# Kernel tuning notes

Measured on AMD Instinct MI355X. Metric: run time of the kernel, lower is better.

Reference implementation:

```python
import jax, jax.numpy as jnp
import numpy as np
from jax import lax

K = 5  # SCNN_KERNEL_LENGTH
PAD = K - 1
PAD_L = PAD // 2
PAD_R = PAD - PAD_L


def setup_inputs() -> dict:
    key = jax.random.key(0)
    k1, k2 = jax.random.split(key)
    B, H, W, C = 16, 256, 256, 32
    inputs = jax.random.normal(k1, (B, H, W, C), dtype=jnp.float32)
    # keras 'random_uniform' init is small; scale randn similarly to keep relu chain stable
    w = jax.random.normal(k2, (C, K, 1, C), dtype=jnp.float32) * 0.05
    b = jnp.zeros((C,), dtype=jnp.float32)
    return {"inputs": inputs, "w": w, "b": b}


def _mvcnn_down(inputs, w, b):
    # inputs: [B,H,W,C]; w: [C,K,1,C] (tf filter: [fh=C, fw=K, in=1, out=C])
    # The tf conv of the transposed row [B,C,W,1] with this filter is exactly a
    # 1D conv over W mixing all C input channels:
    #   out[b,x,o] = sum_{k,c} row_pad[b, x+k, c] * w[c,k,0,o]
    kernel = jnp.transpose(w[:, :, 0, :], (1, 0, 2))  # [K, C_in, C_out]

    def conv_row(x):  # x: [B,W,C] -> [B,W,C]
        return lax.conv_general_dilated(
            x, kernel, window_strides=(1,), padding=[(PAD_L, PAD_R)],
            dimension_numbers=("NWC", "WIO", "NWC"))

    rows = jnp.transpose(inputs, (1, 0, 2, 3))  # [H,B,W,C]

    def step(carry, row):
        # row i of the evolving state = original row + relu-conv result of row i-1
        x = row + carry
        r = jax.nn.relu(conv_row(x) + b)
        return r, r

    init = jnp.zeros_like(rows[0])
    _, out_rows = lax.scan(step, init, rows)  # [H,B,W,C]
    return jnp.transpose(out_rows, (1, 0, 2, 3))  # [B,H,W,C]


def reference(inputs, w, b):
    return _mvcnn_down(inputs, w, b)
```

## Files before the change

### kernel.cpp

```cpp
#include <hip/hip_runtime.h>
#include <stdint.h>

typedef _Float16 f16;
typedef _Float16 f16x2 __attribute__((ext_vector_type(2)));
typedef _Float16 f16x8 __attribute__((ext_vector_type(8)));
typedef float f32x4 __attribute__((ext_vector_type(4)));

#define NB 16
#define NH 256
#define NW 256
#define NC 32
#define NK 5

#define CW 16
#define GC 16
#define XSTR 40
#define XROWS 52

#define FLAG_STRIDE 16
#define MAIL_BASE 4096
#define MAIL_WORDS 256

__device__ __forceinline__ void lds_barrier() {
  asm volatile("s_waitcnt lgkmcnt(0)\n\ts_barrier" ::: "memory");
}

__global__ __launch_bounds__(192, 1)
void mvcnn_down_mb(const float* __restrict__ in, const float* __restrict__ wt,
                   const float* __restrict__ bias, float* __restrict__ out,
                   uint32_t* __restrict__ ws) {
  __shared__ __align__(16) f16 xpad[2][XROWS * XSTR];

  const int bid  = blockIdx.x;
  const int b    = bid & 15;
  const int ck   = bid >> 4;
  const int t    = threadIdx.x;
  const int lane = t & 63;
  const int wv   = t >> 6;
  const int n16  = lane & 15;
  const int q    = lane >> 4;

  const bool act = (wv == 1) || (wv == 0 ? (ck > 0) : (ck < GC - 1));

  f16x8 bfrag[NK][2];
  #pragma unroll
  for (int tap = 0; tap < NK; ++tap) {
    #pragma unroll
    for (int nt = 0; nt < 2; ++nt) {
      f16x8 f;
      #pragma unroll
      for (int j = 0; j < 8; ++j) {
        int cch = q * 4 + (j >> 1) + (j & 1) * 16;
        f[j] = (f16)wt[(cch * NK + tap) * NC + nt * 16 + n16];
      }
      bfrag[tap][nt] = f;
    }
  }
  const float bias0 = bias[n16];
  const float bias1 = bias[16 + n16];

  for (int i = t; i < 2 * XROWS * XSTR; i += 192) (&xpad[0][0])[i] = (f16)0.f;
  __syncthreads();

  const float* inb  = in  + (size_t)b * NH * NW * NC;
  float*       outb = out + (size_t)b * NH * NW * NC;

  const int wo0   = wv * 16 + q * 4;
  const int gcol0 = ck * CW - 16 + wo0;
  const int arow  = wv * 16 + n16;

  uint32_t* flags = ws;
  uint32_t* mail  = ws + MAIL_BASE;
  const int midx  = (q * 4) * 16 + n16;

  float pf0[8], pf1[8];
  auto load_in_row = [&](int h1, float (&pf)[8]) {
    if (!act) return;
    const float* rp = inb + (size_t)h1 * NW * NC;
    #pragma unroll
    for (int r = 0; r < 4; ++r) {
      int g = gcol0 + r;
      pf[2 * r]     = rp[g * NC + n16];
      pf[2 * r + 1] = rp[g * NC + 16 + n16];
    }
  };

  if (act) {
    #pragma unroll
    for (int r = 0; r < 4; ++r) {
      int g = gcol0 + r;
      f16x2 v;
      v[0] = (f16)inb[g * NC + n16];
      v[1] = (f16)inb[g * NC + 16 + n16];
      *(f16x2*)(&xpad[0][(wo0 + r + 2) * XSTR + 2 * n16]) = v;
    }
  }
  load_in_row(1, pf0);
  load_in_row(2, pf1);
  __syncthreads();

  auto body = [&](const int h, float (&pf)[8], f16* xp_cur, f16* xp_nxt) {
    if (h > 0 && (h & 7) == 0) {
      const uint32_t s  = (uint32_t)(h >> 3);
      const int slot    = (int)(s & 1);
      if ((wv == 0 && ck > 0) || (wv == 2 && ck < GC - 1)) {
        const int nb = (wv == 0) ? (bid - GC) : (bid + GC);
        if (lane == 0) {
          while (__hip_atomic_load(&flags[nb * FLAG_STRIDE],
                                   __ATOMIC_RELAXED, __HIP_MEMORY_SCOPE_AGENT) < s)
            __builtin_amdgcn_s_sleep(2);
        }
        asm volatile("" ::: "memory");
        const uint32_t* mb = mail + ((size_t)nb * 2 + slot) * MAIL_WORDS;
        #pragma unroll
        for (int r = 0; r < 4; ++r) {
          uint32_t u = __hip_atomic_load(&mb[midx + r * 16],
                                         __ATOMIC_RELAXED, __HIP_MEMORY_SCOPE_AGENT);
          *(uint32_t*)(&xp_cur[(wo0 + r + 2) * XSTR + 2 * n16]) = u;
        }
      }
      lds_barrier();
    }

    f32x4 acc0 = {0.f, 0.f, 0.f, 0.f};
    f32x4 acc1 = {0.f, 0.f, 0.f, 0.f};
    #pragma unroll
    for (int tap = 0; tap < NK; ++tap) {
      f16x8 af = *(const f16x8*)(xp_cur + (arow + tap) * XSTR + q * 8);
      acc0 = __builtin_amdgcn_mfma_f32_16x16x32_f16(af, bfrag[tap][0], acc0, 0, 0, 0);
      acc1 = __builtin_amdgcn_mfma_f32_16x16x32_f16(af, bfrag[tap][1], acc1, 0, 0, 0);
    }

    float* orow = outb + (size_t)h * NW * NC;
    uint32_t sb[4] = {0, 0, 0, 0};
    #pragma unroll
    for (int r = 0; r < 4; ++r) {
      float y0 = acc0[r] + bias0; y0 = y0 > 0.f ? y0 : 0.f;
      float y1 = acc1[r] + bias1; y1 = y1 > 0.f ? y1 : 0.f;
      if (wv == 1) {
        int g = gcol0 + r;
        orow[g * NC + n16]      = y0;
        orow[g * NC + 16 + n16] = y1;
      }
      if (h < NH - 1 && act) {
        f16x2 v;
        v[0] = (f16)(pf[2 * r]     + y0);
        v[1] = (f16)(pf[2 * r + 1] + y1);
        *(f16x2*)(&xp_nxt[(wo0 + r + 2) * XSTR + 2 * n16]) = v;
        sb[r] = __builtin_bit_cast(uint32_t, v);
      }
    }

    if (((h + 1) & 7) == 0 && (h + 1) < NH && wv == 1) {
      const uint32_t s = (uint32_t)((h + 1) >> 3);
      const int slot   = (int)(s & 1);
      uint32_t* mb = mail + ((size_t)bid * 2 + slot) * MAIL_WORDS;
      #pragma unroll
      for (int r = 0; r < 4; ++r)
        __hip_atomic_store(&mb[midx + r * 16], sb[r],
                           __ATOMIC_RELAXED, __HIP_MEMORY_SCOPE_AGENT);
      asm volatile("s_waitcnt vmcnt(0)" ::: "memory");
      if (lane == 0)
        __hip_atomic_store(&flags[bid * FLAG_STRIDE], s,
                           __ATOMIC_RELAXED, __HIP_MEMORY_SCOPE_AGENT);
    }

    if (h + 3 < NH) load_in_row(h + 3, pf);
    lds_barrier();
  };

  f16* xA = &xpad[0][0];
  f16* xB = &xpad[1][0];
  for (int h = 0; h < NH; h += 2) {
    body(h,     pf0, xA, xB);
    body(h + 1, pf1, xB, xA);
  }
}

__global__ void reset_flags(uint32_t* ws) {
  ws[blockIdx.x * 256 + threadIdx.x] = 0;
}

__global__ __launch_bounds__(1024, 4)
void mvcnn_down(const float* __restrict__ in, const float* __restrict__ wt,
                const float* __restrict__ bias, float* __restrict__ out) {
  __shared__ __align__(16) f16 xpad[2][260 * XSTR];

  const int b    = blockIdx.x;
  const int t    = threadIdx.x;
  const int lane = t & 63;
  const int wv   = t >> 6;
  const int n16  = lane & 15;
  const int q    = lane >> 4;

  f16x8 bfrag[NK][2];
  #pragma unroll
  for (int tap = 0; tap < NK; ++tap) {
    #pragma unroll
    for (int nt = 0; nt < 2; ++nt) {
      f16x8 f;
      #pragma unroll
      for (int j = 0; j < 8; ++j) {
        int cch = q * 4 + (j >> 1) + (j & 1) * 16;
        f[j] = (f16)wt[(cch * NK + tap) * NC + nt * 16 + n16];
      }
      bfrag[tap][nt] = f;
    }
  }
  const float bias0 = bias[n16];
  const float bias1 = bias[16 + n16];

  for (int i = t; i < 2 * 260 * XSTR; i += 1024) (&xpad[0][0])[i] = (f16)0.f;
  __syncthreads();

  const float* inb  = in  + (size_t)b * NH * NW * NC;
  float*       outb = out + (size_t)b * NH * NW * NC;

  const int wo0  = wv * 16 + q * 4;
  const int arow = wv * 16 + n16;

  float pf0[8], pf1[8];
  auto load_in_row = [&](int h1, float (&pf)[8]) {
    const float* rp = inb + (size_t)h1 * NW * NC;
    #pragma unroll
    for (int r = 0; r < 4; ++r) {
      int wo = wo0 + r;
      pf[2 * r]     = rp[wo * NC + n16];
      pf[2 * r + 1] = rp[wo * NC + 16 + n16];
    }
  };

  #pragma unroll
  for (int r = 0; r < 4; ++r) {
    int wo = wo0 + r;
    f16x2 v;
    v[0] = (f16)inb[wo * NC + n16];
    v[1] = (f16)inb[wo * NC + 16 + n16];
    *(f16x2*)(&xpad[0][(wo + 2) * XSTR + 2 * n16]) = v;
  }
  load_in_row(1, pf0);
  load_in_row(2, pf1);
  __syncthreads();

  auto body = [&](const int h, float (&pf)[8], const f16* xp_cur, f16* xp_nxt) {
    f32x4 acc0 = {0.f, 0.f, 0.f, 0.f};
    f32x4 acc1 = {0.f, 0.f, 0.f, 0.f};
    #pragma unroll
    for (int tap = 0; tap < NK; ++tap) {
      f16x8 af = *(const f16x8*)(xp_cur + (arow + tap) * XSTR + q * 8);
      acc0 = __builtin_amdgcn_mfma_f32_16x16x32_f16(af, bfrag[tap][0], acc0, 0, 0, 0);
      acc1 = __builtin_amdgcn_mfma_f32_16x16x32_f16(af, bfrag[tap][1], acc1, 0, 0, 0);
    }
    float* orow = outb + (size_t)h * NW * NC;
    #pragma unroll
    for (int r = 0; r < 4; ++r) {
      float y0 = acc0[r] + bias0; y0 = y0 > 0.f ? y0 : 0.f;
      float y1 = acc1[r] + bias1; y1 = y1 > 0.f ? y1 : 0.f;
      int wo = wo0 + r;
      orow[wo * NC + n16]      = y0;
      orow[wo * NC + 16 + n16] = y1;
      if (h < NH - 1) {
        f16x2 v;
        v[0] = (f16)(pf[2 * r]     + y0);
        v[1] = (f16)(pf[2 * r + 1] + y1);
        *(f16x2*)(&xp_nxt[(wo + 2) * XSTR + 2 * n16]) = v;
      }
    }
    if (h + 3 < NH) load_in_row(h + 3, pf);
    lds_barrier();
  };

  const f16* xA = &xpad[0][0];
  f16* xB = &xpad[1][0];
  for (int h = 0; h < NH; h += 2) {
    body(h,     pf0, xA, xB);
    body(h + 1, pf1, xB, (f16*)xA);
  }
}

extern "C" void kernel_launch(void* const* d_in, const int* in_sizes, int n_in,
                              void* d_out, int out_size, void* d_ws, size_t ws_size,
                              hipStream_t stream) {
  const float* in   = (const float*)d_in[0];
  const float* wt   = (const float*)d_in[1];
  const float* bias = (const float*)d_in[2];
  float* out = (float*)d_out;

  const size_t need = (size_t)(MAIL_BASE + 256 * 2 * MAIL_WORDS) * 4;
  if (d_ws != nullptr && ws_size >= need) {
    hipLaunchKernelGGL(reset_flags, dim3(16), dim3(256), 0, stream, (uint32_t*)d_ws);
    hipLaunchKernelGGL(mvcnn_down_mb, dim3(NB * GC), dim3(192), 0, stream,
                       in, wt, bias, out, (uint32_t*)d_ws);
  } else {
    hipLaunchKernelGGL(mvcnn_down, dim3(NB), dim3(1024), 0, stream,
                       in, wt, bias, out);
  }
}
```

Measured before the change: 377.5 us.

## Compute two rows per barrier with widened halo and key-tagged flags

Each even-row step now computes a wider halo of outputs (two extra MFMA tiles per wave), so the following odd row can be built entirely from data the same wave wrote. That removes one LDS barrier per pair of rows. LDS goes to triple buffering, and input prefetch is split into wide and narrow loads. Neighbour-exchange flags become per-slot tags derived from the step index, which removes the separate flag-reset kernel launch. In exchange the even rows do redundant boundary compute and the control logic is more complex.

Measured after the change: 936.8 us. 2.48x slower.

```diff
diff --git a/kernel.cpp b/kernel.cpp
--- a/kernel.cpp
+++ b/kernel.cpp
@@ -15,11 +15,13 @@
 #define CW 16
 #define GC 16
 #define XSTR 40
-#define XROWS 52
-
-#define FLAG_STRIDE 16
-#define MAIL_BASE 4096
+#define XROWS 56
+
+#define FLAG_U32 16
+#define NFLAGS (NB * GC * 2 * FLAG_U32)
+#define MAIL_BASE NFLAGS
 #define MAIL_WORDS 256
+#define KEYOF(k) (0x5EED0000u ^ (uint32_t)(k))
 
 __device__ __forceinline__ void lds_barrier() {
   asm volatile("s_waitcnt lgkmcnt(0)\n\ts_barrier" ::: "memory");
@@ -29,7 +31,7 @@
 void mvcnn_down_mb(const float* __restrict__ in, const float* __restrict__ wt,
                    const float* __restrict__ bias, float* __restrict__ out,
                    uint32_t* __restrict__ ws) {
-  __shared__ __align__(16) f16 xpad[2][XROWS * XSTR];
+  __shared__ __align__(16) f16 xpad[3][XROWS * XSTR];
 
   const int bid  = blockIdx.x;
   const int b    = bid & 15;
@@ -59,7 +61,7 @@
   const float bias0 = bias[n16];
   const float bias1 = bias[16 + n16];
 
-  for (int i = t; i < 2 * XROWS * XSTR; i += 192) (&xpad[0][0])[i] = (f16)0.f;
+  for (int i = t; i < 3 * XROWS * XSTR; i += 192) (&xpad[0][0])[i] = (f16)0.f;
   __syncthreads();
 
   const float* inb  = in  + (size_t)b * NH * NW * NC;
@@ -73,15 +75,36 @@
   uint32_t* mail  = ws + MAIL_BASE;
   const int midx  = (q * 4) * 16 + n16;
 
-  float pf0[8], pf1[8];
-  auto load_in_row = [&](int h1, float (&pf)[8]) {
-    if (!act) return;
+  float pW1[2][8], pW0[2][8], pN[2][8];
+
+  auto load_narrow = [&](int h1, float (&pf)[8]) {
+    if (!act || h1 >= NH) return;
     const float* rp = inb + (size_t)h1 * NW * NC;
     #pragma unroll
     for (int r = 0; r < 4; ++r) {
       int g = gcol0 + r;
       pf[2 * r]     = rp[g * NC + n16];
       pf[2 * r + 1] = rp[g * NC + 16 + n16];
+    }
+  };
+  auto load_wide = [&](int h1, float (&pT1)[8], float (&pT0)[8]) {
+    if (!act || h1 >= NH) return;
+    const float* rp = inb + (size_t)h1 * NW * NC;
+    #pragma unroll
+    for (int r = 0; r < 4; ++r) {
+      int g1 = gcol0 + 2 + r;
+      int gc = g1 < NW ? g1 : NW - 1;
+      pT1[2 * r]     = rp[gc * NC + n16];
+      pT1[2 * r + 1] = rp[gc * NC + 16 + n16];
+    }
+    if (q == 0) {
+      #pragma unroll
+      for (int r = 0; r < 4; ++r) {
+        int g0 = gcol0 - 2 + r;
+        int gc = g0 > 0 ? g0 : 0;
+        pT0[2 * r]     = rp[gc * NC + n16];
+        pT0[2 * r + 1] = rp[gc * NC + 16 + n16];
+      }
     }
   };
 
@@ -92,93 +115,147 @@
       f16x2 v;
       v[0] = (f16)inb[g * NC + n16];
       v[1] = (f16)inb[g * NC + 16 + n16];
-      *(f16x2*)(&xpad[0][(wo0 + r + 2) * XSTR + 2 * n16]) = v;
-    }
-  }
-  load_in_row(1, pf0);
-  load_in_row(2, pf1);
+      *(f16x2*)(&xpad[0][(wo0 + r + 4) * XSTR + 2 * n16]) = v;
+    }
+  }
+  load_wide(1, pW1[0], pW0[0]);
+  load_narrow(2, pN[0]);
   __syncthreads();
 
-  auto body = [&](const int h, float (&pf)[8], f16* xp_cur, f16* xp_nxt) {
+  auto body_even = [&](const int h, float (&pT1)[8], float (&pT0)[8],
+                       f16* xp_cur, f16* xp_nxt) {
     if (h > 0 && (h & 7) == 0) {
-      const uint32_t s  = (uint32_t)(h >> 3);
-      const int slot    = (int)(s & 1);
+      const int k = h >> 3;
+      const int ms = k & 1;
       if ((wv == 0 && ck > 0) || (wv == 2 && ck < GC - 1)) {
         const int nb = (wv == 0) ? (bid - GC) : (bid + GC);
         if (lane == 0) {
-          while (__hip_atomic_load(&flags[nb * FLAG_STRIDE],
-                                   __ATOMIC_RELAXED, __HIP_MEMORY_SCOPE_AGENT) < s)
-            __builtin_amdgcn_s_sleep(2);
+          while (__hip_atomic_load(&flags[(nb * 2 + ms) * FLAG_U32],
+                                   __ATOMIC_RELAXED, __HIP_MEMORY_SCOPE_AGENT)
+                 != KEYOF(k))
+            __builtin_amdgcn_s_sleep(1);
         }
         asm volatile("" ::: "memory");
-        const uint32_t* mb = mail + ((size_t)nb * 2 + slot) * MAIL_WORDS;
+        const uint32_t* mb = mail + ((size_t)nb * 2 + ms) * MAIL_WORDS;
         #pragma unroll
         for (int r = 0; r < 4; ++r) {
           uint32_t u = __hip_atomic_load(&mb[midx + r * 16],
                                          __ATOMIC_RELAXED, __HIP_MEMORY_SCOPE_AGENT);
-          *(uint32_t*)(&xp_cur[(wo0 + r + 2) * XSTR + 2 * n16]) = u;
+          *(uint32_t*)(&xp_cur[(wo0 + r + 4) * XSTR + 2 * n16]) = u;
         }
       }
       lds_barrier();
     }
 
-    f32x4 acc0 = {0.f, 0.f, 0.f, 0.f};
-    f32x4 acc1 = {0.f, 0.f, 0.f, 0.f};
+    f32x4 a00 = {bias0, bias0, bias0, bias0};
+    f32x4 a01 = {bias1, bias1, bias1, bias1};
+    f32x4 a10 = a00, a11 = a01;
     #pragma unroll
     for (int tap = 0; tap < NK; ++tap) {
-      f16x8 af = *(const f16x8*)(xp_cur + (arow + tap) * XSTR + q * 8);
+      f16x8 f0 = *(const f16x8*)(xp_cur + (arow + tap) * XSTR + q * 8);
+      f16x8 f1 = *(const f16x8*)(xp_cur + (arow + tap + 4) * XSTR + q * 8);
+      a00 = __builtin_amdgcn_mfma_f32_16x16x32_f16(f0, bfrag[tap][0], a00, 0, 0, 0);
+      a01 = __builtin_amdgcn_mfma_f32_16x16x32_f16(f0, bfrag[tap][1], a01, 0, 0, 0);
+      a10 = __builtin_amdgcn_mfma_f32_16x16x32_f16(f1, bfrag[tap][0], a10, 0, 0, 0);
+      a11 = __builtin_amdgcn_mfma_f32_16x16x32_f16(f1, bfrag[tap][1], a11, 0, 0, 0);
+    }
+
+    float* orow = outb + (size_t)h * NW * NC;
+    #pragma unroll
+    for (int r = 0; r < 4; ++r) {
+      float y00 = fmaxf(a00[r], 0.f), y01 = fmaxf(a01[r], 0.f);
+      float y10 = fmaxf(a10[r], 0.f), y11 = fmaxf(a11[r], 0.f);
+      const int g1 = gcol0 + 2 + r;
+      const int g0 = gcol0 - 2 + r;
+      if (wv == 1) {
+        if (q * 4 + r <= 13) {
+          orow[g1 * NC + n16]      = y10;
+          orow[g1 * NC + 16 + n16] = y11;
+        }
+        if (q == 0 && r >= 2) {
+          orow[g0 * NC + n16]      = y00;
+          orow[g0 * NC + 16 + n16] = y01;
+        }
+      }
+      if (h < NH - 1 && act) {
+        if ((unsigned)g1 < NW) {
+          f16x2 v;
+          v[0] = (f16)(pT1[2 * r]     + y10);
+          v[1] = (f16)(pT1[2 * r + 1] + y11);
+          *(f16x2*)(&xp_nxt[(wv * 16 + 6 + q * 4 + r) * XSTR + 2 * n16]) = v;
+        }
+        if (q == 0 && (unsigned)g0 < NW) {
+          f16x2 v;
+          v[0] = (f16)(pT0[2 * r]     + y00);
+          v[1] = (f16)(pT0[2 * r + 1] + y01);
+          *(f16x2*)(&xp_nxt[(wv * 16 + 2 + r) * XSTR + 2 * n16]) = v;
+        }
+      }
+    }
+  };
+
+  auto body_odd = [&](const int h, float (&pf)[8], f16* xp_cur, f16* xp_nxt) {
+    f32x4 acc0 = {bias0, bias0, bias0, bias0};
+    f32x4 acc1 = {bias1, bias1, bias1, bias1};
+    #pragma unroll
+    for (int tap = 0; tap < NK; ++tap) {
+      f16x8 af = *(const f16x8*)(xp_cur + (arow + tap + 2) * XSTR + q * 8);
       acc0 = __builtin_amdgcn_mfma_f32_16x16x32_f16(af, bfrag[tap][0], acc0, 0, 0, 0);
       acc1 = __builtin_amdgcn_mfma_f32_16x16x32_f16(af, bfrag[tap][1], acc1, 0, 0, 0);
     }
 
-    float* orow = outb + (size_t)h * NW * NC;
     uint32_t sb[4] = {0, 0, 0, 0};
-    #pragma unroll
-    for (int r = 0; r < 4; ++r) {
-      float y0 = acc0[r] + bias0; y0 = y0 > 0.f ? y0 : 0.f;
-      float y1 = acc1[r] + bias1; y1 = y1 > 0.f ? y1 : 0.f;
-      if (wv == 1) {
-        int g = gcol0 + r;
-        orow[g * NC + n16]      = y0;
-        orow[g * NC + 16 + n16] = y1;
-      }
+    float y0v[4], y1v[4];
+    #pragma unroll
+    for (int r = 0; r < 4; ++r) {
+      float y0 = fmaxf(acc0[r], 0.f);
+      float y1 = fmaxf(acc1[r], 0.f);
+      y0v[r] = y0; y1v[r] = y1;
       if (h < NH - 1 && act) {
         f16x2 v;
         v[0] = (f16)(pf[2 * r]     + y0);
         v[1] = (f16)(pf[2 * r + 1] + y1);
-        *(f16x2*)(&xp_nxt[(wo0 + r + 2) * XSTR + 2 * n16]) = v;
+        *(f16x2*)(&xp_nxt[(wo0 + r + 4) * XSTR + 2 * n16]) = v;
         sb[r] = __builtin_bit_cast(uint32_t, v);
       }
     }
 
     if (((h + 1) & 7) == 0 && (h + 1) < NH && wv == 1) {
-      const uint32_t s = (uint32_t)((h + 1) >> 3);
-      const int slot   = (int)(s & 1);
-      uint32_t* mb = mail + ((size_t)bid * 2 + slot) * MAIL_WORDS;
+      const int k = (h + 1) >> 3;
+      const int ms = k & 1;
+      uint32_t* mb = mail + ((size_t)bid * 2 + ms) * MAIL_WORDS;
       #pragma unroll
       for (int r = 0; r < 4; ++r)
         __hip_atomic_store(&mb[midx + r * 16], sb[r],
                            __ATOMIC_RELAXED, __HIP_MEMORY_SCOPE_AGENT);
       asm volatile("s_waitcnt vmcnt(0)" ::: "memory");
       if (lane == 0)
-        __hip_atomic_store(&flags[bid * FLAG_STRIDE], s,
+        __hip_atomic_store(&flags[(bid * 2 + ms) * FLAG_U32], KEYOF(k),
                            __ATOMIC_RELAXED, __HIP_MEMORY_SCOPE_AGENT);
     }
 
-    if (h + 3 < NH) load_in_row(h + 3, pf);
+    if (wv == 1) {
+      float* orow = outb + (size_t)h * NW * NC;
+      #pragma unroll
+      for (int r = 0; r < 4; ++r) {
+        const int g = gcol0 + r;
+        orow[g * NC + n16]      = y0v[r];
+        orow[g * NC + 16 + n16] = y1v[r];
+      }
+    }
+  };
+
+  for (int h = 0; h < NH; h += 2) {
+    const int it = (h >> 1) & 1;
+    f16* bA = &xpad[h % 3][0];
+    f16* bB = &xpad[(h + 1) % 3][0];
+    f16* bC = &xpad[(h + 2) % 3][0];
+    body_even(h, pW1[it], pW0[it], bA, bB);
+    load_wide(h + 3, pW1[it ^ 1], pW0[it ^ 1]);
+    body_odd(h + 1, pN[it], bB, bC);
+    load_narrow(h + 4, pN[it ^ 1]);
     lds_barrier();
-  };
-
-  f16* xA = &xpad[0][0];
-  f16* xB = &xpad[1][0];
-  for (int h = 0; h < NH; h += 2) {
-    body(h,     pf0, xA, xB);
-    body(h + 1, pf1, xB, xA);
-  }
-}
-
-__global__ void reset_flags(uint32_t* ws) {
-  ws[blockIdx.x * 256 + threadIdx.x] = 0;
+  }
 }
 
 __global__ __launch_bounds__(1024, 4)
@@ -286,9 +363,8 @@
   const float* bias = (const float*)d_in[2];
   float* out = (float*)d_out;
 
-  const size_t need = (size_t)(MAIL_BASE + 256 * 2 * MAIL_WORDS) * 4;
+  const size_t need = (size_t)(NFLAGS + NB * GC * 2 * MAIL_WORDS) * 4;
   if (d_ws != nullptr && ws_size >= need) {
-    hipLaunchKernelGGL(reset_flags, dim3(16), dim3(256), 0, stream, (uint32_t*)d_ws);
     hipLaunchKernelGGL(mvcnn_down_mb, dim3(NB * GC), dim3(192), 0, stream,
                        in, wt, bias, out, (uint32_t*)d_ws);
   } else {
```

## Split width into 32 chunks of 8 columns with two-neighbor halo exchange

Applied to the files above, without the earlier changes.

Each batch image is now split across 32 blocks, each owning 8 output columns instead of 16, which doubles the block count to 512 and allows two blocks per CU. Because the halo of 16 columns now spans two neighbours on each side, the exchange reads mailboxes from two blocks per side. The flags carry a per-step key with double-buffered slots, so the separate reset kernel launch is removed. This trades more redundant halo computation and more cross-block synchronisation for finer parallelism and one fewer launch. The sentinel-key scheme assumes stale workspace contents never happen to match a key.

After: 418.4 us. 1.11x slower.

```diff
diff --git a/kernel.cpp b/kernel.cpp
--- a/kernel.cpp
+++ b/kernel.cpp
@@ -12,20 +12,23 @@
 #define NC 32
 #define NK 5
 
-#define CW 16
-#define GC 16
+#define OWN 8
+#define GC 32
+#define NBLK (NB * GC)
 #define XSTR 40
-#define XROWS 52
-
-#define FLAG_STRIDE 16
-#define MAIL_BASE 4096
-#define MAIL_WORDS 256
+#define XROWS 44
+
+#define FLAG_U32 16
+#define NFLAGS (NBLK * 2 * FLAG_U32)
+#define MAIL_BASE NFLAGS
+#define MAIL_WORDS 128
+#define KEYOF(k) (0x5EED0000u ^ (uint32_t)(k))
 
 __device__ __forceinline__ void lds_barrier() {
   asm volatile("s_waitcnt lgkmcnt(0)\n\ts_barrier" ::: "memory");
 }
 
-__global__ __launch_bounds__(192, 1)
+__global__ __launch_bounds__(192, 2)
 void mvcnn_down_mb(const float* __restrict__ in, const float* __restrict__ wt,
                    const float* __restrict__ bias, float* __restrict__ out,
                    uint32_t* __restrict__ ws) {
@@ -40,7 +43,7 @@
   const int n16  = lane & 15;
   const int q    = lane >> 4;
 
-  const bool act = (wv == 1) || (wv == 0 ? (ck > 0) : (ck < GC - 1));
+  const int TB = (wv == 0) ? 0 : (wv == 1 ? 16 : 24);
 
   f16x8 bfrag[NK][2];
   #pragma unroll
@@ -65,120 +68,138 @@
   const float* inb  = in  + (size_t)b * NH * NW * NC;
   float*       outb = out + (size_t)b * NH * NW * NC;
 
-  const int wo0   = wv * 16 + q * 4;
-  const int gcol0 = ck * CW - 16 + wo0;
-  const int arow  = wv * 16 + n16;
+  const int cl0 = TB + q * 4;
+  const int g0  = ck * OWN - 16 + cl0;
+  const int arow = TB + n16;
 
   uint32_t* flags = ws;
   uint32_t* mail  = ws + MAIL_BASE;
-  const int midx  = (q * 4) * 16 + n16;
+
+  const int  rsrc   = (wv == 0) ? (q < 2 ? ck - 2 : ck - 1)
+                                : (q < 2 ? ck + 1 : ck + 2);
+  const bool rvalid = (wv != 1) && ((unsigned)rsrc < GC);
+  const int  rmidx  = ((q & 1) * 4) * 16 + n16;
+  const int  smidx  = (q * 4) * 16 + n16;
 
   float pf0[8], pf1[8];
-  auto load_in_row = [&](int h1, float (&pf)[8]) {
-    if (!act) return;
+  auto load_row = [&](int h1, float (&pf)[8]) {
+    if (h1 >= NH) return;
     const float* rp = inb + (size_t)h1 * NW * NC;
     #pragma unroll
     for (int r = 0; r < 4; ++r) {
-      int g = gcol0 + r;
-      pf[2 * r]     = rp[g * NC + n16];
-      pf[2 * r + 1] = rp[g * NC + 16 + n16];
+      int g  = g0 + r;
+      int gc = g < 0 ? 0 : (g > NW - 1 ? NW - 1 : g);
+      pf[2 * r]     = rp[gc * NC + n16];
+      pf[2 * r + 1] = rp[gc * NC + 16 + n16];
     }
   };
 
-  if (act) {
-    #pragma unroll
-    for (int r = 0; r < 4; ++r) {
-      int g = gcol0 + r;
+  #pragma unroll
+  for (int r = 0; r < 4; ++r) {
+    int g = g0 + r;
+    if ((unsigned)g < NW) {
       f16x2 v;
       v[0] = (f16)inb[g * NC + n16];
       v[1] = (f16)inb[g * NC + 16 + n16];
-      *(f16x2*)(&xpad[0][(wo0 + r + 2) * XSTR + 2 * n16]) = v;
-    }
-  }
-  load_in_row(1, pf0);
-  load_in_row(2, pf1);
+      *(f16x2*)(&xpad[0][(cl0 + r + 2) * XSTR + 2 * n16]) = v;
+    }
+  }
+  load_row(1, pf0);
+  load_row(2, pf1);
   __syncthreads();
 
-  auto body = [&](const int h, float (&pf)[8], f16* xp_cur, f16* xp_nxt) {
+  auto body = [&](const int h, float (&pf)[8], f16* xc, f16* xn) {
     if (h > 0 && (h & 7) == 0) {
-      const uint32_t s  = (uint32_t)(h >> 3);
-      const int slot    = (int)(s & 1);
-      if ((wv == 0 && ck > 0) || (wv == 2 && ck < GC - 1)) {
-        const int nb = (wv == 0) ? (bid - GC) : (bid + GC);
-        if (lane == 0) {
-          while (__hip_atomic_load(&flags[nb * FLAG_STRIDE],
-                                   __ATOMIC_RELAXED, __HIP_MEMORY_SCOPE_AGENT) < s)
-            __builtin_amdgcn_s_sleep(2);
+      const int k  = h >> 3;
+      const int ms = k & 1;
+      if (wv != 1) {
+        if (lane < 2) {
+          int sc = (wv == 0) ? (ck - 1 - lane) : (ck + 1 + lane);
+          if ((unsigned)sc < GC) {
+            const int sbid = sc * 16 + b;
+            while (__hip_atomic_load(&flags[(sbid * 2 + ms) * FLAG_U32],
+                                     __ATOMIC_RELAXED, __HIP_MEMORY_SCOPE_AGENT)
+                   != KEYOF(k))
+              __builtin_amdgcn_s_sleep(2);
+          }
         }
         asm volatile("" ::: "memory");
-        const uint32_t* mb = mail + ((size_t)nb * 2 + slot) * MAIL_WORDS;
-        #pragma unroll
-        for (int r = 0; r < 4; ++r) {
-          uint32_t u = __hip_atomic_load(&mb[midx + r * 16],
-                                         __ATOMIC_RELAXED, __HIP_MEMORY_SCOPE_AGENT);
-          *(uint32_t*)(&xp_cur[(wo0 + r + 2) * XSTR + 2 * n16]) = u;
+        if (rvalid) {
+          const uint32_t* mb =
+              mail + ((size_t)(rsrc * 16 + b) * 2 + ms) * MAIL_WORDS;
+          #pragma unroll
+          for (int r = 0; r < 4; ++r) {
+            uint32_t u = __hip_atomic_load(&mb[rmidx + r * 16],
+                                           __ATOMIC_RELAXED,
+                                           __HIP_MEMORY_SCOPE_AGENT);
+            *(uint32_t*)(&xc[(cl0 + r + 2) * XSTR + 2 * n16]) = u;
+          }
         }
       }
       lds_barrier();
     }
 
-    f32x4 acc0 = {0.f, 0.f, 0.f, 0.f};
-    f32x4 acc1 = {0.f, 0.f, 0.f, 0.f};
+    f32x4 acc0 = {bias0, bias0, bias0, bias0};
+    f32x4 acc1 = {bias1, bias1, bias1, bias1};
     #pragma unroll
     for (int tap = 0; tap < NK; ++tap) {
-      f16x8 af = *(const f16x8*)(xp_cur + (arow + tap) * XSTR + q * 8);
+      f16x8 af = *(const f16x8*)(xc + (arow + tap) * XSTR + q * 8);
       acc0 = __builtin_amdgcn_mfma_f32_16x16x32_f16(af, bfrag[tap][0], acc0, 0, 0, 0);
       acc1 = __builtin_amdgcn_mfma_f32_16x16x32_f16(af, bfrag[tap][1], acc1, 0, 0, 0);
     }
 
-    float* orow = outb + (size_t)h * NW * NC;
     uint32_t sb[4] = {0, 0, 0, 0};
+    float y0v[4], y1v[4];
     #pragma unroll
     for (int r = 0; r < 4; ++r) {
-      float y0 = acc0[r] + bias0; y0 = y0 > 0.f ? y0 : 0.f;
-      float y1 = acc1[r] + bias1; y1 = y1 > 0.f ? y1 : 0.f;
-      if (wv == 1) {
-        int g = gcol0 + r;
-        orow[g * NC + n16]      = y0;
-        orow[g * NC + 16 + n16] = y1;
-      }
-      if (h < NH - 1 && act) {
+      float y0 = fmaxf(acc0[r], 0.f);
+      float y1 = fmaxf(acc1[r], 0.f);
+      y0v[r] = y0; y1v[r] = y1;
+      int g = g0 + r;
+      if (h < NH - 1 && (unsigned)g < NW) {
         f16x2 v;
         v[0] = (f16)(pf[2 * r]     + y0);
         v[1] = (f16)(pf[2 * r + 1] + y1);
-        *(f16x2*)(&xp_nxt[(wo0 + r + 2) * XSTR + 2 * n16]) = v;
+        *(f16x2*)(&xn[(cl0 + r + 2) * XSTR + 2 * n16]) = v;
         sb[r] = __builtin_bit_cast(uint32_t, v);
       }
     }
 
-    if (((h + 1) & 7) == 0 && (h + 1) < NH && wv == 1) {
-      const uint32_t s = (uint32_t)((h + 1) >> 3);
-      const int slot   = (int)(s & 1);
-      uint32_t* mb = mail + ((size_t)bid * 2 + slot) * MAIL_WORDS;
-      #pragma unroll
-      for (int r = 0; r < 4; ++r)
-        __hip_atomic_store(&mb[midx + r * 16], sb[r],
-                           __ATOMIC_RELAXED, __HIP_MEMORY_SCOPE_AGENT);
+    const bool sendrow = (((h + 1) & 7) == 0) && (h + 1 < NH);
+    if (sendrow && wv == 1) {
+      const int k  = (h + 1) >> 3;
+      const int ms = k & 1;
+      if (q < 2) {
+        uint32_t* mb = mail + ((size_t)bid * 2 + ms) * MAIL_WORDS;
+        #pragma unroll
+        for (int r = 0; r < 4; ++r)
+          __hip_atomic_store(&mb[smidx + r * 16], sb[r],
+                             __ATOMIC_RELAXED, __HIP_MEMORY_SCOPE_AGENT);
+      }
       asm volatile("s_waitcnt vmcnt(0)" ::: "memory");
       if (lane == 0)
-        __hip_atomic_store(&flags[bid * FLAG_STRIDE], s,
+        __hip_atomic_store(&flags[(bid * 2 + ms) * FLAG_U32], KEYOF(k),
                            __ATOMIC_RELAXED, __HIP_MEMORY_SCOPE_AGENT);
     }
 
-    if (h + 3 < NH) load_in_row(h + 3, pf);
+    if (wv == 1 && q < 2) {
+      float* orow = outb + (size_t)h * NW * NC;
+      #pragma unroll
+      for (int r = 0; r < 4; ++r) {
+        const int g = g0 + r;
+        orow[g * NC + n16]      = y0v[r];
+        orow[g * NC + 16 + n16] = y1v[r];
+      }
+    }
+
+    load_row(h + 3, pf);
     lds_barrier();
   };
 
-  f16* xA = &xpad[0][0];
-  f16* xB = &xpad[1][0];
   for (int h = 0; h < NH; h += 2) {
-    body(h,     pf0, xA, xB);
-    body(h + 1, pf1, xB, xA);
-  }
-}
-
-__global__ void reset_flags(uint32_t* ws) {
-  ws[blockIdx.x * 256 + threadIdx.x] = 0;
+    body(h,     pf0, &xpad[0][0], &xpad[1][0]);
+    body(h + 1, pf1, &xpad[1][0], &xpad[0][0]);
+  }
 }
 
 __global__ __launch_bounds__(1024, 4)
@@ -286,10 +307,9 @@
   const float* bias = (const float*)d_in[2];
   float* out = (float*)d_out;
 
-  const size_t need = (size_t)(MAIL_BASE + 256 * 2 * MAIL_WORDS) * 4;
+  const size_t need = (size_t)(NFLAGS + NBLK * 2 * MAIL_WORDS) * 4;
   if (d_ws != nullptr && ws_size >= need) {
-    hipLaunchKernelGGL(reset_flags, dim3(16), dim3(256), 0, stream, (uint32_t*)d_ws);
-    hipLaunchKernelGGL(mvcnn_down_mb, dim3(NB * GC), dim3(192), 0, stream,
+    hipLaunchKernelGGL(mvcnn_down_mb, dim3(NBLK), dim3(192), 0, stream,
                        in, wt, bias, out, (uint32_t*)d_ws);
   } else {
     hipLaunchKernelGGL(mvcnn_down, dim3(NB), dim3(1024), 0, stream,
```
